# Kernel optimization log

Measured on AMD Instinct MI355X. Metric: run time of the kernel, lower is better.

Reference implementation:

```python
import jax, jax.numpy as jnp
import numpy as np

B, T, D = 4, 4096, 384
H = W = 64
K = 8            # num_clusters
CH = MH = 64     # conv_hidden, mlp_hidden
NL = 4           # num_layers
IN_DIM = D + 2   # use_spatial_pos
RADIUS_FRACTION = 30.0
GRAPH_EPS = 1e-6
SM_LAMBDA = 0.01
FS_LAMBDA = 0.09


def conv2d(x, w, b, groups=1):
    out = jax.lax.conv_general_dilated(x, w, (1, 1), 'SAME',
        dimension_numbers=('NCHW', 'OIHW', 'NCHW'), feature_group_count=groups)
    return out + b[None, :, None, None]


def group_norm(x, g, b, groups, eps=1e-5):
    n, c, h, w = x.shape
    xg = x.reshape(n, groups, c // groups, h, w)
    m = xg.mean(axis=(2, 3, 4), keepdims=True)
    v = xg.var(axis=(2, 3, 4), keepdims=True)
    xn = ((xg - m) * jax.lax.rsqrt(v + eps)).reshape(n, c, h, w)
    return xn * g[None, :, None, None] + b[None, :, None, None]


def layer_norm(x, g, b, eps=1e-5):
    m = x.mean(-1, keepdims=True)
    v = x.var(-1, keepdims=True)
    return (x - m) * jax.lax.rsqrt(v + eps) * g + b


def build_graph():
    # unit-square grid positions; radius graph with self loops; sym normalization
    lin = jnp.linspace(0.0, 1.0, H)
    gy, gx = jnp.meshgrid(lin, lin, indexing='ij')
    pos = jnp.stack([gx.reshape(-1), gy.reshape(-1)], axis=1)  # (T,2)
    r2 = 2.0 / (RADIUS_FRACTION * RADIUS_FRACTION)             # (sqrt(2)/rf)^2
    dx = pos[:, 0][:, None] - pos[:, 0][None, :]
    dy = pos[:, 1][:, None] - pos[:, 1][None, :]
    adj = ((dx * dx + dy * dy) <= r2).astype(jnp.float32)      # includes loop
    deg = adj.sum(1)
    dis = jnp.where(deg > 0, deg ** -0.5, 0.0)
    a_tilde = dis[:, None] * adj * dis[None, :]                # D^-1/2 A D^-1/2
    return pos, a_tilde


def setup_inputs():
    key = jax.random.key(0)
    ks = jax.random.split(key, 16)
    rn = lambda i, s, sc=0.05: jax.random.normal(ks[i], s, dtype=jnp.float32) * sc
    z = lambda s: jnp.zeros(s, jnp.float32)
    o = lambda s: jnp.ones(s, jnp.float32)
    return {
        'token_features': jax.random.normal(ks[0], (B, T, D), dtype=jnp.float32),
        'gcn_w0': rn(1, (IN_DIM, CH)), 'gcn_b0': z((CH,)),
        'gcn_w': rn(2, (NL - 1, CH, CH)), 'gcn_b': z((NL - 1, CH)),
        'ln_g': o((NL, CH)), 'ln_b': z((NL, CH)),
        'res_w': rn(3, (IN_DIM, CH)), 'res_b': z((CH,)),
        'res_ln_g': o((CH,)), 'res_ln_b': z((CH,)),
        'mlp_w1': rn(4, (CH, MH)), 'mlp_b1': z((MH,)),
        'mlp_ln_g': o((MH,)), 'mlp_ln_b': z((MH,)),
        'mlp_w2': rn(5, (MH, K)), 'mlp_b2': z((K,)),
        'sm_w1': rn(6, (K, 1, 3, 3)), 'sm_b1': z((K,)),
        'sm_gn1_g': o((K,)), 'sm_gn1_b': z((K,)),
        'sm_w2': rn(7, (K, 1, 3, 3)), 'sm_b2': z((K,)),
        'sm_gn2_g': o((K,)), 'sm_gn2_b': z((K,)),
        'ec_w1': rn(8, (32, D, 3, 3), 0.02), 'ec_b1': z((32,)),
        'ec_gn_g': o((32,)), 'ec_gn_b': z((32,)),
        'ec_w2': rn(9, (1, 32, 1, 1)), 'ec_b2': z((1,)),
        'k': 8,
    }


def reference(token_features, gcn_w0, gcn_b0, gcn_w, gcn_b, ln_g, ln_b,
              res_w, res_b, res_ln_g, res_ln_b, mlp_w1, mlp_b1, mlp_ln_g,
              mlp_ln_b, mlp_w2, mlp_b2, sm_w1, sm_b1, sm_gn1_g, sm_gn1_b,
              sm_w2, sm_b2, sm_gn2_g, sm_gn2_b, ec_w1, ec_b1, ec_gn_g,
              ec_gn_b, ec_w2, ec_b2, k):
    pos, A = build_graph()

    # ---- feature smoothness loss (edge-aware) ----
    fs = token_features.reshape(B, H, W, D).transpose(0, 3, 1, 2)  # (B,D,H,W)
    e = jax.nn.relu(group_norm(conv2d(fs, ec_w1, ec_b1), ec_gn_g, ec_gn_b, 8))
    ew = jax.nn.sigmoid(conv2d(e, ec_w2, ec_b2))                   # (B,1,H,W)
    gy = fs[:, :, 1:, :] - fs[:, :, :-1, :]
    gx = fs[:, :, :, 1:] - fs[:, :, :, :-1]
    loss_y = (gy * gy * ew[:, :, 1:, :]).mean() / D
    loss_x = (gx * gx * ew[:, :, :, 1:]).mean() / D
    feat_sm = (loss_y + loss_x) / 2

    # ---- GNN pool (batched; adjacency shared across batch) ----
    x = jnp.concatenate(
        [token_features, jnp.broadcast_to(pos[None], (B, T, 2))], axis=-1)
    Ws = [gcn_w0] + [gcn_w[i] for i in range(NL - 1)]
    bs = [gcn_b0] + [gcn_b[i] for i in range(NL - 1)]
    for i in range(NL):
        x_prev = x
        h = jnp.einsum('ts,bsc->btc', A, x @ Ws[i]) + bs[i]  # GCNConv
        h = jax.nn.elu(layer_norm(h, ln_g[i], ln_b[i]))
        if i == 0:
            x_prev = layer_norm(x_prev @ res_w + res_b, res_ln_g, res_ln_b)
        x = h + x_prev
    h1 = jax.nn.elu(layer_norm(x @ mlp_w1 + mlp_b1, mlp_ln_g, mlp_ln_b))
    S = jax.nn.softmax(h1 @ mlp_w2 + mlp_b2, axis=-1)        # (B,T,K)

    # ---- spatial smoothness loss (depthwise convs) ----
    S_sp = S.transpose(0, 2, 1).reshape(B, K, H, W)
    t = jax.nn.relu(group_norm(conv2d(S_sp, sm_w1, sm_b1, groups=K),
                               sm_gn1_g, sm_gn1_b, K))
    S_sm = group_norm(conv2d(t, sm_w2, sm_b2, groups=K), sm_gn2_g, sm_gn2_b, K)
    sm_loss = ((S_sm - S_sp) ** 2).mean(axis=(1, 2, 3))      # (B,)

    # ---- normalized-cut + orthogonality losses ----
    AS = jnp.einsum('ts,bsk->btk', A, S)
    num = jnp.einsum('btk,btk->b', S, AS)
    degA = A.sum(1)
    den = jnp.einsum('btk,t,btk->b', S, degA, S) + GRAPH_EPS
    loss_c = -num / den
    SS = jnp.einsum('btk,btl->bkl', S, S)
    ssn = jnp.sqrt((SS * SS).sum(axis=(1, 2)))
    eyeK = jnp.eye(K, dtype=jnp.float32)
    target = eyeK / (jnp.sqrt(jnp.float32(K)) + GRAPH_EPS)
    diff = SS / (ssn[:, None, None] + GRAPH_EPS) - target[None]
    loss_o = jnp.sqrt((diff * diff).sum(axis=(1, 2)))

    loss = (loss_c + loss_o + SM_LAMBDA * sm_loss).mean() + FS_LAMBDA * feat_sm
    return S, loss
```

## Files before the change

### kernel.cpp

```cpp
#include <hip/hip_runtime.h>
#include <hip/hip_bf16.h>


#define B_ 4
#define T_ 4096
#define D_ 384

typedef __attribute__((ext_vector_type(8))) short short8b;
typedef __attribute__((ext_vector_type(4))) float f32x4;

__device__ __forceinline__ float wred(float v) {
#pragma unroll
  for (int off = 32; off > 0; off >>= 1) v += __shfl_xor(v, off);
  return v;
}

__device__ __forceinline__ void wred2(float& a, float& b) {
#pragma unroll
  for (int off = 32; off > 0; off >>= 1) {
    a += __shfl_xor(a, off);
    b += __shfl_xor(b, off);
  }
}

__device__ __forceinline__ short bf16rne(float f) {
  unsigned u = __float_as_uint(f);
  unsigned r = (u + 0x7FFFu + ((u >> 16) & 1u)) >> 16;
  return (short)r;
}

__device__ __forceinline__ float bf2f(short s) {
  return __uint_as_float(((unsigned)(unsigned short)s) << 16);
}

__device__ __forceinline__ float uval(int i) {
  int c = (i < 2 ? i : 2) + ((63 - i) < 2 ? (63 - i) : 2) + 1;
  return rsqrtf((float)c);
}

struct PGcn {
  const float *feat, *ecw1, *w0, *resw, *resb, *resg, *reslb;
  const float *gw, *gb0, *gb, *lng, *lnb;
  const float *w1, *b1, *mlng, *mlnb, *w2, *b2;
  short *fb, *wq, *wb;
  float *accg, *xwA, *xwB, *xbuf, *resbuf, *S, *Sp;
};

struct PLoss {
  const float *S, *Sp;
  const float *smw1, *smb1, *smg1, *smbb1, *smw2, *smb2, *smg2, *smbb2;
  const short *fb, *wq;
  const float *ecb1;
  float *eraw, *accg;
  const float *gng, *gnb, *ecw2, *ecb2;
  float *ew, *outp;
};


__device__ __forceinline__ void prep_stage(int blk, int tid,
    const float* feat, const float* ecw1, const float* w0, const float* resw,
    short* fb, short* wq, short* wb, float* accg) {
  if (blk == 0) {
    accg[tid] = 0.f;
    accg[tid + 256] = 0.f;
  }
  if (blk < 3072) {
    int t = blk * 256 + tid;
    const float4* s = (const float4*)feat + (size_t)t * 2;
    float4 a = s[0], b = s[1];
    short8b v;
    v[0] = bf16rne(a.x); v[1] = bf16rne(a.y); v[2] = bf16rne(a.z); v[3] = bf16rne(a.w);
    v[4] = bf16rne(b.x); v[5] = bf16rne(b.y); v[6] = bf16rne(b.z); v[7] = bf16rne(b.w);
    *(short8b*)(fb + (size_t)t * 8) = v;
  } else if (blk < 3504) {
    int idx = (blk - 3072) * 256 + tid;
    int q = idx % 9;
    int rest = idx / 9;
    int d = rest % 384;
    int o = rest / 384;
    wq[((size_t)(q * 32 + o)) * 384 + d] = bf16rne(ecw1[idx]);
  } else {
    int u = (blk - 3504) * 256 + tid;
    int l = u & 63, f = (u >> 6) & 7, s = u >> 9;
    int c = f * 16 + (l & 15);
    int k0 = s * 32 + ((l >> 4) << 3);
    const float* src = (c < 64) ? (w0 + c) : (resw + (c - 64));
    short8b v;
#pragma unroll
    for (int j = 0; j < 8; ++j) v[j] = bf16rne(src[(size_t)(k0 + j) * 64]);
    *(short8b*)(wb + (size_t)u * 8) = v;
  }
}

__device__ __forceinline__ void gemm0_stage(char* smem, int blk, int tid,
    const short* fb, const short* wb, const float* w0, const float* resw,
    const float* resb, const float* resg, const float* reslb,
    float* xw, float* res) {
  short8b* Ab8 = (short8b*)smem;
  int row0 = blk * 32;
#pragma unroll
  for (int it = 0; it < 6; ++it) {
    int u = it * 256 + tid;
    int l = u & 63, s = (u >> 6) % 12, set = u / 768;
    int row = row0 + set * 16 + (l & 15);
    int k = s * 32 + ((l >> 4) << 3);
    Ab8[(set * 12 + s) * 64 + l] = *(const short8b*)(fb + (size_t)row * 384 + k);
  }
  __syncthreads();
  int wid = tid >> 6, lane = tid & 63;
  int rowset = wid & 1, colhalf = wid >> 1;
  const short8b* wb8 = (const short8b*)wb;
  f32x4 acc[4];
#pragma unroll
  for (int f = 0; f < 4; ++f) acc[f] = (f32x4){0.f, 0.f, 0.f, 0.f};
#pragma unroll
  for (int s = 0; s < 12; ++s) {
    short8b av = Ab8[(rowset * 12 + s) * 64 + lane];
#pragma unroll
    for (int f = 0; f < 4; ++f) {
      short8b bv = wb8[((size_t)(s * 8 + colhalf * 4 + f)) * 64 + lane];
      acc[f] = __builtin_amdgcn_mfma_f32_16x16x32_bf16(av, bv, acc[f], 0, 0, 0);
    }
  }
  int g = lane >> 4, ln = lane & 15;
  if (colhalf == 0) {
    float pw1[4], pw2[4];
#pragma unroll
    for (int f = 0; f < 4; ++f) {
      int c = f * 16 + ln;
      pw1[f] = w0[384 * 64 + c];
      pw2[f] = w0[385 * 64 + c];
    }
#pragma unroll
    for (int r = 0; r < 4; ++r) {
      int grow = row0 + rowset * 16 + g * 4 + r;
      int t = grow & (T_ - 1);
      float px = (float)(t & 63) * (1.f / 63.f);
      float py = (float)(t >> 6) * (1.f / 63.f);
#pragma unroll
      for (int f = 0; f < 4; ++f)
        xw[(size_t)grow * 64 + f * 16 + ln] = acc[f][r] + px * pw1[f] + py * pw2[f];
    }
  } else {
    float rw1[4], rw2[4], rb[4], rgam[4], rbet[4];
#pragma unroll
    for (int f = 0; f < 4; ++f) {
      int c = f * 16 + ln;
      rw1[f] = resw[384 * 64 + c];
      rw2[f] = resw[385 * 64 + c];
      rb[f] = resb[c]; rgam[f] = resg[c]; rbet[f] = reslb[c];
    }
#pragma unroll
    for (int r = 0; r < 4; ++r) {
      int grow = row0 + rowset * 16 + g * 4 + r;
      int t = grow & (T_ - 1);
      float px = (float)(t & 63) * (1.f / 63.f);
      float py = (float)(t >> 6) * (1.f / 63.f);
      float rv[4];
      float s1 = 0.f, s2 = 0.f;
#pragma unroll
      for (int f = 0; f < 4; ++f) {
        float v = acc[f][r] + px * rw1[f] + py * rw2[f] + rb[f];
        rv[f] = v;
        s1 += v;
        s2 = fmaf(v, v, s2);
      }
#pragma unroll
      for (int off = 1; off < 16; off <<= 1) {
        s1 += __shfl_xor(s1, off);
        s2 += __shfl_xor(s2, off);
      }
      float mean = s1 * (1.f / 64.f);
      float var = s2 * (1.f / 64.f) - mean * mean;
      float inv = rsqrtf(var + 1e-5f);
#pragma unroll
      for (int f = 0; f < 4; ++f)
        res[(size_t)grow * 64 + f * 16 + ln] =
            (rv[f] - mean) * inv * rgam[f] + rbet[f];
    }
  }
}

__device__ __forceinline__ void layer_stage(char* smem, int blk, int tid,
    const float* xw_in, const float* W, const float* bias, const float* lng,
    const float* lnb, const float* resid, float* xout, float* xw_out) {
  float* sx = (float*)smem;
  float* sW = (float*)(smem + 4096);
  int t0 = blk * 16;
  int b = t0 >> 12, i = (t0 >> 6) & 63;
  const float4* w4 = (const float4*)W;
  float4* sW4 = (float4*)sW;
#pragma unroll
  for (int l = 0; l < 4; ++l) sW4[tid + l * 256] = w4[tid + l * 256];
  int c = tid & 63, jg = tid >> 6;
  int jb = (t0 & 63) + jg * 4;
  float ui = uval(i);
  float acc[4];
#pragma unroll
  for (int m = 0; m < 4; ++m) acc[m] = 0.f;
  float uw[8];
#pragma unroll
  for (int d = 0; d < 8; ++d) {
    int jj = jb - 2 + d;
    uw[d] = (jj >= 0 && jj < 64) ? uval(jj) : 0.f;
  }
#pragma unroll
  for (int di = -2; di <= 2; ++di) {
    int ii = i + di;
    if (ii < 0 || ii > 63) continue;
    float wi = uval(ii);
    const float* src = xw_in + ((size_t)((b << 12) + (ii << 6))) * 64 + c;
    float v[8];
#pragma unroll
    for (int d = 0; d < 8; ++d) {
      int jj = jb - 2 + d;
      v[d] = (jj >= 0 && jj < 64) ? src[jj * 64] : 0.f;
    }
#pragma unroll
    for (int m = 0; m < 4; ++m) {
      float t = v[m] * uw[m] + v[m + 1] * uw[m + 1] + v[m + 2] * uw[m + 2] +
                v[m + 3] * uw[m + 3] + v[m + 4] * uw[m + 4];
      acc[m] = fmaf(wi, t, acc[m]);
    }
  }
  float bc = bias[c], gam = lng[c], bet = lnb[c];
#pragma unroll
  for (int m = 0; m < 4; ++m) {
    int lrow = jg * 4 + m;
    float h = ui * uval(jb + m) * acc[m] + bc;
    float s1 = h, s2 = h * h;
    wred2(s1, s2);
    float mean = s1 * (1.f / 64.f);
    float var = s2 * (1.f / 64.f) - mean * mean;
    float n = (h - mean) * rsqrtf(var + 1e-5f) * gam + bet;
    float e = n > 0.f ? n : (expf(n) - 1.f);
    float xv = e + resid[(size_t)(t0 + lrow) * 64 + c];
    xout[(size_t)(t0 + lrow) * 64 + c] = xv;
    sx[lrow * 64 + c] = xv;
  }
  __syncthreads();
  float a[4];
#pragma unroll
  for (int m = 0; m < 4; ++m) a[m] = 0.f;
#pragma unroll
  for (int kq = 0; kq < 16; ++kq) {
    float4 fv[4];
#pragma unroll
    for (int m = 0; m < 4; ++m)
      fv[m] = *(const float4*)&sx[(jg * 4 + m) * 64 + kq * 4];
#pragma unroll
    for (int dk = 0; dk < 4; ++dk) {
      float wv = sW[(kq * 4 + dk) * 64 + c];
#pragma unroll
      for (int m = 0; m < 4; ++m)
        a[m] = fmaf(((const float*)&fv[m])[dk], wv, a[m]);
    }
  }
#pragma unroll
  for (int m = 0; m < 4; ++m)
    xw_out[(size_t)(t0 + jg * 4 + m) * 64 + c] = a[m];
}

__device__ __forceinline__ void st4mlp_stage(char* smem, int blk, int tid,
    const float* xw_in, const float* bias, const float* lng, const float* lnb,
    const float* resid, const float* w1, const float* b1, const float* mlng,
    const float* mlnb, const float* w2, const float* b2, float* S, float* Sp) {
  float* sx = (float*)smem;
  float* sW = (float*)(smem + 8192);
  float* sh = (float*)(smem + 24576);
  int t0 = blk * 32;
  int b = t0 >> 12, i = (t0 >> 6) & 63;
  const float4* w4 = (const float4*)w1;
  float4* sW4 = (float4*)sW;
#pragma unroll
  for (int l = 0; l < 4; ++l) sW4[tid + l * 256] = w4[tid + l * 256];
  int c = tid & 63, jg = tid >> 6;
  int jb = (t0 & 63) + jg * 8;
  float ui = uval(i);
  float acc[8];
#pragma unroll
  for (int m = 0; m < 8; ++m) acc[m] = 0.f;
  float uw[12];
#pragma unroll
  for (int d = 0; d < 12; ++d) {
    int jj = jb - 2 + d;
    uw[d] = (jj >= 0 && jj < 64) ? uval(jj) : 0.f;
  }
#pragma unroll
  for (int di = -2; di <= 2; ++di) {
    int ii = i + di;
    if (ii < 0 || ii > 63) continue;
    float wi = uval(ii);
    const float* src = xw_in + ((size_t)((b << 12) + (ii << 6))) * 64 + c;
    float v[12];
#pragma unroll
    for (int d = 0; d < 12; ++d) {
      int jj = jb - 2 + d;
      v[d] = (jj >= 0 && jj < 64) ? src[jj * 64] : 0.f;
    }
#pragma unroll
    for (int m = 0; m < 8; ++m) {
      float t = v[m] * uw[m] + v[m + 1] * uw[m + 1] + v[m + 2] * uw[m + 2] +
                v[m + 3] * uw[m + 3] + v[m + 4] * uw[m + 4];
      acc[m] = fmaf(wi, t, acc[m]);
    }
  }
  float bc = bias[c], gam = lng[c], bet = lnb[c];
#pragma unroll
  for (int m = 0; m < 8; ++m) {
    int lrow = jg * 8 + m;
    float h = ui * uval(jb + m) * acc[m] + bc;
    float s1 = h, s2 = h * h;
    wred2(s1, s2);
    float mean = s1 * (1.f / 64.f);
    float var = s2 * (1.f / 64.f) - mean * mean;
    float n = (h - mean) * rsqrtf(var + 1e-5f) * gam + bet;
    float e = n > 0.f ? n : (expf(n) - 1.f);
    sx[lrow * 64 + c] = e + resid[(size_t)(t0 + lrow) * 64 + c];
  }
  __syncthreads();
  float a[8];
#pragma unroll
  for (int m = 0; m < 8; ++m) a[m] = 0.f;
#pragma unroll
  for (int kq = 0; kq < 16; ++kq) {
    float4 fv[8];
#pragma unroll
    for (int m = 0; m < 8; ++m)
      fv[m] = *(const float4*)&sx[(jg * 8 + m) * 64 + kq * 4];
#pragma unroll
    for (int dk = 0; dk < 4; ++dk) {
      float wv = sW[(kq * 4 + dk) * 64 + c];
#pragma unroll
      for (int m = 0; m < 8; ++m)
        a[m] = fmaf(((const float*)&fv[m])[dk], wv, a[m]);
    }
  }
  float mb = b1[c], mgam = mlng[c], mbet = mlnb[c];
#pragma unroll
  for (int m = 0; m < 8; ++m) {
    float h = a[m] + mb;
    float s1 = h, s2 = h * h;
    wred2(s1, s2);
    float mean = s1 * (1.f / 64.f);
    float var = s2 * (1.f / 64.f) - mean * mean;
    float n = (h - mean) * rsqrtf(var + 1e-5f) * mgam + mbet;
    sh[(jg * 8 + m) * 64 + c] = n > 0.f ? n : (expf(n) - 1.f);
  }
  __syncthreads();
  int k = tid & 7, j = tid >> 3;
  float lg = b2[k];
#pragma unroll 8
  for (int u = 0; u < 64; ++u) {
    int cc = (u + j * 8) & 63;
    lg = fmaf(sh[j * 64 + cc], w2[cc * 8 + k], lg);
  }
  float mx = lg;
  mx = fmaxf(mx, __shfl_xor(mx, 1));
  mx = fmaxf(mx, __shfl_xor(mx, 2));
  mx = fmaxf(mx, __shfl_xor(mx, 4));
  float ex = expf(lg - mx);
  float sum = ex;
  sum += __shfl_xor(sum, 1);
  sum += __shfl_xor(sum, 2);
  sum += __shfl_xor(sum, 4);
  float val = ex / sum;
  int grow = t0 + j;
  int t = grow & (T_ - 1);
  S[(size_t)grow * 8 + k] = val;
  Sp[((size_t)((b << 3) + k) << 12) + t] = val;
}

__device__ __forceinline__ void cut_stage(char* smem, int blk, int tid,
    const float* S, float* accg) {
  {
    int k = tid & 7;
    int tl = tid >> 3;
    int gid = blk * 32 + tl;
    int b = gid >> 12, t = gid & (T_ - 1);
    int i = t >> 6, j = t & 63;
    float ui = uval(i), uj = uval(j);
    float as = 0.f, sui = 0.f, suj = 0.f;
#pragma unroll
    for (int di = -2; di <= 2; ++di) {
      int ii = i + di;
      if (ii < 0 || ii > 63) continue;
      float wi = uval(ii);
      sui += wi;
#pragma unroll
      for (int dj = -2; dj <= 2; ++dj) {
        int jj = j + dj;
        if (jj < 0 || jj > 63) continue;
        as = fmaf(wi * uval(jj),
                  S[((size_t)((b << 12) + (ii << 6) + jj)) * 8 + k], as);
      }
    }
#pragma unroll
    for (int dj = -2; dj <= 2; ++dj) {
      int jj = j + dj;
      if (jj >= 0 && jj <= 63) suj += uval(jj);
    }
    as *= ui * uj;
    float sv = S[(size_t)gid * 8 + k];
    float degA = ui * uj * sui * suj;
    float numv = sv * as, denv = sv * sv * degA;
    wred2(numv, denv);
    float* lds = (float*)smem;
    int wid = tid >> 6, lane = tid & 63;
    if (lane == 0) { lds[wid * 2] = numv; lds[wid * 2 + 1] = denv; }
    __syncthreads();
    if (tid == 0) {
      int slot = b * 4 + (blk & 3);
      atomicAdd(&accg[slot], lds[0] + lds[2] + lds[4] + lds[6]);
      atomicAdd(&accg[16 + slot], lds[1] + lds[3] + lds[5] + lds[7]);
    }
  }
  if (blk < 32) {
    __syncthreads();
    int b = blk >> 3, chunk = blk & 7;
    int wid = tid >> 6, lane = tid & 63;
    int kk = lane >> 3, ll = lane & 7;
    int t0 = chunk * 512 + wid * 128;
    float a = 0.f;
    const float* Sb = S + ((size_t)b << 12) * 8;
    for (int it = 0; it < 128; ++it) {
      const float* sr = Sb + (size_t)(t0 + it) * 8;
      a = fmaf(sr[kk], sr[ll], a);
    }
    float* lds2 = (float*)smem;
    lds2[tid] = a;
    __syncthreads();
    if (tid < 64) {
      float s = lds2[tid] + lds2[tid + 64] + lds2[tid + 128] + lds2[tid + 192];
      atomicAdd(&accg[128 + b * 64 + tid], s);
    }
  }
}

__device__ __forceinline__ void sm_stage(char* smem, int bk, int tid,
    const float* Sp, const float* w1, const float* b1, const float* g1,
    const float* bb1, const float* w2, const float* b2, const float* g2,
    const float* bb2, float* accg) {
  float* p0 = (float*)smem;
  float* p1 = p0 + 4096;
  float* red = p1 + 4096;
  int b = bk >> 3, k = bk & 7;
  const float4* src = (const float4*)(Sp + (size_t)bk * 4096);
  float4* d0 = (float4*)p0;
  for (int i2 = tid; i2 < 1024; i2 += 256) d0[i2] = src[i2];
  float W1[9], W2[9];
#pragma unroll
  for (int q = 0; q < 9; ++q) { W1[q] = w1[k * 9 + q]; W2[q] = w2[k * 9 + q]; }
  __syncthreads();
  int wid = tid >> 6, lane = tid & 63;
  float y[16];
  float s1 = 0.f, s2 = 0.f;
#pragma unroll
  for (int v = 0; v < 16; ++v) {
    int p = v * 256 + tid;
    int i2 = p >> 6, j2 = p & 63;
    float a = b1[k];
#pragma unroll
    for (int dy = 0; dy < 3; ++dy) {
      int ii = i2 + dy - 1;
      if (ii < 0 || ii > 63) continue;
#pragma unroll
      for (int dx = 0; dx < 3; ++dx) {
        int jj = j2 + dx - 1;
        if (jj < 0 || jj > 63) continue;
        a = fmaf(W1[dy * 3 + dx], p0[(ii << 6) + jj], a);
      }
    }
    y[v] = a;
    s1 += a;
    s2 = fmaf(a, a, s2);
  }
  wred2(s1, s2);
  if (lane == 0) { red[wid * 2] = s1; red[wid * 2 + 1] = s2; }
  __syncthreads();
  float mean = (red[0] + red[2] + red[4] + red[6]) * (1.f / 4096.f);
  float var = (red[1] + red[3] + red[5] + red[7]) * (1.f / 4096.f) - mean * mean;
  float inv = rsqrtf(var + 1e-5f) * g1[k];
  float sh = bb1[k];
  __syncthreads();
#pragma unroll
  for (int v = 0; v < 16; ++v) {
    int p = v * 256 + tid;
    p1[p] = fmaxf((y[v] - mean) * inv + sh, 0.f);
  }
  __syncthreads();
  s1 = 0.f; s2 = 0.f;
#pragma unroll
  for (int v = 0; v < 16; ++v) {
    int p = v * 256 + tid;
    int i2 = p >> 6, j2 = p & 63;
    float a = b2[k];
#pragma unroll
    for (int dy = 0; dy < 3; ++dy) {
      int ii = i2 + dy - 1;
      if (ii < 0 || ii > 63) continue;
#pragma unroll
      for (int dx = 0; dx < 3; ++dx) {
        int jj = j2 + dx - 1;
        if (jj < 0 || jj > 63) continue;
        a = fmaf(W2[dy * 3 + dx], p1[(ii << 6) + jj], a);
      }
    }
    y[v] = a;
    s1 += a;
    s2 = fmaf(a, a, s2);
  }
  wred2(s1, s2);
  if (lane == 0) { red[wid * 2] = s1; red[wid * 2 + 1] = s2; }
  __syncthreads();
  float mean2 = (red[0] + red[2] + red[4] + red[6]) * (1.f / 4096.f);
  float var2 = (red[1] + red[3] + red[5] + red[7]) * (1.f / 4096.f) - mean2 * mean2;
  float inv2 = rsqrtf(var2 + 1e-5f) * g2[k];
  float sh2 = bb2[k];
  float sd = 0.f;
#pragma unroll
  for (int v = 0; v < 16; ++v) {
    int p = v * 256 + tid;
    float sm = (y[v] - mean2) * inv2 + sh2;
    float dd = sm - p0[p];
    sd = fmaf(dd, dd, sd);
  }
  sd = wred(sd);
  __syncthreads();
  if (lane == 0) red[wid] = sd;
  __syncthreads();
  if (tid == 0)
    atomicAdd(&accg[384 + b * 2 + (bk & 1)],
              (red[0] + red[1] + red[2] + red[3]) * (1.f / 32768.f));
}

__device__ __forceinline__ void ecconv_stage(char* smem, int blk2, int tid,
    const short* fb, const short* wq, const float* ecb1, float* eraw,
    float* accg) {
  short* Abuf = (short*)smem;
  short* Wbuf = Abuf + 8040;
  float* sW1 = (float*)smem;
  float* sW2 = sW1 + 128;
  int b = blk2 >> 6, i = blk2 & 63;
  int wid = tid >> 6, lane = tid & 63;
  int m = lane & 15, kg = lane >> 4;
  if (tid < 36) {
    int zkg = tid & 3, sl = (tid >> 2) % 3, r = tid / 12;
    int slot = sl == 0 ? 0 : (sl == 1 ? 65 : 66);
    *(short8b*)&Abuf[(r * 67 + slot) * 40 + zkg * 8] = (short8b)0;
  }
  f32x4 acc0 = {0.f, 0.f, 0.f, 0.f};
  f32x4 acc1 = {0.f, 0.f, 0.f, 0.f};
  int abase = (wid * 16 + m) * 40 + kg * 8;
  int bbase = m * 40 + kg * 8;
  for (int c = 0; c < 12; ++c) {
    __syncthreads();
#pragma unroll
    for (int s = 0; s < 3; ++s) {
      int cid = tid + (s << 8);
      int akg = cid & 3, px = (cid >> 2) & 63, r = cid >> 8;
      int ii = i + r - 1;
      short8b v = (short8b)0;
      if (ii >= 0 && ii < 64)
        v = *(const short8b*)(fb +
              ((size_t)((b << 12) + (ii << 6) + px)) * D_ + c * 32 + akg * 8);
      *(short8b*)&Abuf[(r * 67 + px + 1) * 40 + akg * 8] = v;
    }
    for (int l = tid; l < 1152; l += 256) {
      int wkg = l & 3, oo = (l >> 2) & 31, q = l >> 7;
      short8b wv =
          *(const short8b*)(wq + ((size_t)(q * 32 + oo)) * D_ + c * 32 + wkg * 8);
      *(short8b*)&Wbuf[(q * 32 + oo) * 40 + wkg * 8] = wv;
    }
    __syncthreads();
#pragma unroll
    for (int q = 0; q < 9; ++q) {
      short8b av = *(const short8b*)&Abuf[abase + ((q / 3) * 67 + (q % 3)) * 40];
      short8b bv0 = *(const short8b*)&Wbuf[bbase + q * 1280];
      short8b bv1 = *(const short8b*)&Wbuf[bbase + q * 1280 + 640];
      acc0 = __builtin_amdgcn_mfma_f32_16x16x32_bf16(av, bv0, acc0, 0, 0, 0);
      acc1 = __builtin_amdgcn_mfma_f32_16x16x32_bf16(av, bv1, acc1, 0, 0, 0);
    }
  }
  __syncthreads();
  int o0 = m, o1 = 16 + m;
  float bs0 = ecb1[o0], bs1 = ecb1[o1];
  float s1a = 0.f, s2a = 0.f, s1b = 0.f, s2b = 0.f;
  int jbase = wid * 16 + kg * 4;
#pragma unroll
  for (int rg = 0; rg < 4; ++rg) {
    float v0 = acc0[rg] + bs0;
    float v1 = acc1[rg] + bs1;
    int j = jbase + rg;
    size_t px = ((size_t)((b << 12) + (i << 6) + j)) * 32;
    eraw[px + o0] = v0;
    eraw[px + o1] = v1;
    s1a += v0; s2a = fmaf(v0, v0, s2a);
    s1b += v1; s2b = fmaf(v1, v1, s2b);
  }
  s1a += __shfl_xor(s1a, 16); s1a += __shfl_xor(s1a, 32);
  s2a += __shfl_xor(s2a, 16); s2a += __shfl_xor(s2a, 32);
  s1b += __shfl_xor(s1b, 16); s1b += __shfl_xor(s1b, 32);
  s2b += __shfl_xor(s2b, 16); s2b += __shfl_xor(s2b, 32);
  if (lane < 16) {
    sW1[wid * 32 + lane] = s1a; sW2[wid * 32 + lane] = s2a;
    sW1[wid * 32 + lane + 16] = s1b; sW2[wid * 32 + lane + 16] = s2b;
  }
  __syncthreads();
  if (tid < 32) {
    float t1 = sW1[tid] + sW1[32 + tid] + sW1[64 + tid] + sW1[96 + tid];
    float t2 = sW2[tid] + sW2[32 + tid] + sW2[64 + tid] + sW2[96 + tid];
    t1 += __shfl_xor(t1, 1); t1 += __shfl_xor(t1, 2);
    t2 += __shfl_xor(t2, 1); t2 += __shfl_xor(t2, 2);
    if ((tid & 3) == 0) {
      atomicAdd(&accg[64 + b * 16 + (tid >> 2) * 2], t1);
      atomicAdd(&accg[64 + b * 16 + (tid >> 2) * 2 + 1], t2);
    }
  }
}

__device__ __forceinline__ void ecfinal_stage(char* smem, int blk, int tid,
    const float* eraw, const float* accg, const float* gng, const float* gnb,
    const float* w2, const float* b2, float* ew) {
  float* st = (float*)smem;
  int idx = blk * 256 + tid;
  int b = idx >> 12;
  if (tid < 16) st[tid] = accg[64 + b * 16 + tid];
  __syncthreads();
  float a = b2[0];
  const float4* er = (const float4*)(eraw + (size_t)idx * 32);
#pragma unroll
  for (int oq = 0; oq < 8; ++oq) {
    float mean = st[oq * 2] * (1.f / 16384.f);
    float var = st[oq * 2 + 1] * (1.f / 16384.f) - mean * mean;
    float inv = rsqrtf(var + 1e-5f);
    float4 e = er[oq];
    int o = oq * 4;
    float v0 = (e.x - mean) * inv * gng[o + 0] + gnb[o + 0];
    float v1 = (e.y - mean) * inv * gng[o + 1] + gnb[o + 1];
    float v2 = (e.z - mean) * inv * gng[o + 2] + gnb[o + 2];
    float v3 = (e.w - mean) * inv * gng[o + 3] + gnb[o + 3];
    a = fmaf(fmaxf(v0, 0.f), w2[o + 0], a);
    a = fmaf(fmaxf(v1, 0.f), w2[o + 1], a);
    a = fmaf(fmaxf(v2, 0.f), w2[o + 2], a);
    a = fmaf(fmaxf(v3, 0.f), w2[o + 3], a);
  }
  ew[idx] = 1.f / (1.f + expf(-a));
}

__device__ __forceinline__ void fsloss_stage(char* smem, int blk, int tid,
    const short* fb, const float* ew, float* accg) {
  float sy = 0.f, sx = 0.f;
  const int N = B_ * T_ * 48;
  for (int idx = blk * 256 + tid; idx < N; idx += 512 * 256) {
    int d8 = idx % 48;
    int rt = idx / 48;
    int t = rt & (T_ - 1);
    int i = t >> 6, j = t & 63;
    const short8b* fp = (const short8b*)(fb + (size_t)rt * D_) + d8;
    short8b f0 = *fp;
    if (i < 63) {
      short8b f1 = fp[64 * 48];
      float w = ew[rt + 64];
      float a = 0.f;
#pragma unroll
      for (int u = 0; u < 8; ++u) {
        float d = bf2f(f1[u]) - bf2f(f0[u]);
        a = fmaf(d, d, a);
      }
      sy += w * a;
    }
    if (j < 63) {
      short8b f1 = fp[48];
      float w = ew[rt + 1];
      float a = 0.f;
#pragma unroll
      for (int u = 0; u < 8; ++u) {
        float d = bf2f(f1[u]) - bf2f(f0[u]);
        a = fmaf(d, d, a);
      }
      sx += w * a;
    }
  }
  wred2(sy, sx);
  float* lds = (float*)smem;
  int wid = tid >> 6, lane = tid & 63;
  if (lane == 0) { lds[wid * 2] = sy; lds[wid * 2 + 1] = sx; }
  __syncthreads();
  if (tid == 0) {
    int slot = 32 + (blk & 15) * 2;
    atomicAdd(&accg[slot], lds[0] + lds[2] + lds[4] + lds[6]);
    atomicAdd(&accg[slot + 1], lds[1] + lds[3] + lds[5] + lds[7]);
  }
}

__device__ __forceinline__ void final_stage(const float* accg, float* out) {
  float total = 0.f;
  for (int b = 0; b < 4; ++b) {
    const float* SSb = accg + 128 + b * 64;
    float ssq = 0.f;
    for (int v = 0; v < 64; ++v) ssq += SSb[v] * SSb[v];
    float ssn = sqrtf(ssq);
    float tgt = 1.f / (sqrtf(8.f) + 1e-6f);
    float inv = 1.f / (ssn + 1e-6f);
    float lo = 0.f;
    for (int kk = 0; kk < 8; ++kk)
      for (int ll = 0; ll < 8; ++ll) {
        float dd = SSb[kk * 8 + ll] * inv - (kk == ll ? tgt : 0.f);
        lo += dd * dd;
      }
    lo = sqrtf(lo);
    float num = accg[b * 4] + accg[b * 4 + 1] + accg[b * 4 + 2] + accg[b * 4 + 3];
    float den = accg[16 + b * 4] + accg[16 + b * 4 + 1] + accg[16 + b * 4 + 2] +
                accg[16 + b * 4 + 3];
    float lc = -num / (den + 1e-6f);
    float smv = accg[384 + b * 2] + accg[385 + b * 2];
    total += lc + lo + 0.01f * smv;
  }
  total *= 0.25f;
  float fsy = 0.f, fsx = 0.f;
  for (int s = 0; s < 16; ++s) { fsy += accg[32 + s * 2]; fsx += accg[33 + s * 2]; }
  const float cnt = 4.f * 384.f * 63.f * 64.f;
  float ly = fsy / cnt * (1.f / 384.f);
  float lx = fsx / cnt * (1.f / 384.f);
  out[131072] = total + 0.09f * 0.5f * (ly + lx);
}


__global__ __launch_bounds__(256) void k_prep(PGcn p) {
  prep_stage(blockIdx.x, threadIdx.x, p.feat, p.ecw1, p.w0, p.resw, p.fb, p.wq,
             p.wb, p.accg);
}

__global__ __launch_bounds__(256) void k_mix1(PGcn g, PLoss l) {
  __shared__ __align__(16) char smem[39168];
  if (blockIdx.x < 256) {
    int lb = (blockIdx.x & 7) * 32 + (blockIdx.x >> 3);
    ecconv_stage(smem, lb, threadIdx.x, l.fb, l.wq, l.ecb1, l.eraw, l.accg);
  } else {
    gemm0_stage(smem, blockIdx.x - 256, threadIdx.x, g.fb, g.wb, g.w0, g.resw,
                g.resb, g.resg, g.reslb, g.xwA, g.resbuf);
  }
}

__global__ __launch_bounds__(256) void k_mix2(PGcn g, PLoss l) {
  __shared__ __align__(16) char smem[20480];
  if (blockIdx.x < 64)
    ecfinal_stage(smem, blockIdx.x, threadIdx.x, l.eraw, l.accg, l.gng, l.gnb,
                  l.ecw2, l.ecb2, l.ew);
  else
    layer_stage(smem, blockIdx.x - 64, threadIdx.x, g.xwA, g.gw, g.gb0, g.lng,
                g.lnb, g.resbuf, g.xbuf, g.xwB);
}

__global__ __launch_bounds__(256) void k_mix3(PGcn g, PLoss l) {
  __shared__ __align__(16) char smem[20480];
  if (blockIdx.x < 512)
    fsloss_stage(smem, blockIdx.x, threadIdx.x, l.fb, l.ew, l.accg);
  else
    layer_stage(smem, blockIdx.x - 512, threadIdx.x, g.xwB, g.gw + 4096, g.gb,
                g.lng + 64, g.lnb + 64, g.xbuf, g.xbuf, g.xwA);
}

__global__ __launch_bounds__(256) void k_layer2(PGcn p) {
  __shared__ __align__(16) char smem[20480];
  layer_stage(smem, blockIdx.x, threadIdx.x, p.xwA, p.gw + 8192, p.gb + 64,
              p.lng + 128, p.lnb + 128, p.xbuf, p.xbuf, p.xwB);
}

__global__ __launch_bounds__(256) void k_st4mlp(PGcn p) {
  __shared__ __align__(16) char smem[32768];
  st4mlp_stage(smem, blockIdx.x, threadIdx.x, p.xwB, p.gb + 128, p.lng + 192,
               p.lnb + 192, p.xbuf, p.w1, p.b1, p.mlng, p.mlnb, p.w2, p.b2,
               p.S, p.Sp);
}

__global__ __launch_bounds__(256) void k_cutsm(PLoss p) {
  __shared__ __align__(16) char smem[32832];
  if (blockIdx.x < 512)
    cut_stage(smem, blockIdx.x, threadIdx.x, p.S, p.accg);
  else
    sm_stage(smem, blockIdx.x - 512, threadIdx.x, p.Sp, p.smw1, p.smb1, p.smg1,
             p.smbb1, p.smw2, p.smb2, p.smg2, p.smbb2, p.accg);
}

__global__ void k_final(PLoss p) {
  if (threadIdx.x == 0 && blockIdx.x == 0) final_stage(p.accg, p.outp);
}


extern "C" void kernel_launch(void* const* d_in, const int* in_sizes, int n_in,
                              void* d_out, int out_size, void* d_ws, size_t ws_size,
                              hipStream_t stream) {
  const float* feat = (const float*)d_in[0];
  const float* gcn_w0 = (const float*)d_in[1];
  const float* gcn_b0 = (const float*)d_in[2];
  const float* gcn_w = (const float*)d_in[3];
  const float* gcn_b = (const float*)d_in[4];
  const float* ln_g = (const float*)d_in[5];
  const float* ln_b = (const float*)d_in[6];
  const float* res_w = (const float*)d_in[7];
  const float* res_b = (const float*)d_in[8];
  const float* res_ln_g = (const float*)d_in[9];
  const float* res_ln_b = (const float*)d_in[10];
  const float* mlp_w1 = (const float*)d_in[11];
  const float* mlp_b1 = (const float*)d_in[12];
  const float* mlp_ln_g = (const float*)d_in[13];
  const float* mlp_ln_b = (const float*)d_in[14];
  const float* mlp_w2 = (const float*)d_in[15];
  const float* mlp_b2 = (const float*)d_in[16];
  const float* sm_w1 = (const float*)d_in[17];
  const float* sm_b1 = (const float*)d_in[18];
  const float* sm_g1 = (const float*)d_in[19];
  const float* sm_bb1 = (const float*)d_in[20];
  const float* sm_w2 = (const float*)d_in[21];
  const float* sm_b2 = (const float*)d_in[22];
  const float* sm_g2 = (const float*)d_in[23];
  const float* sm_bb2 = (const float*)d_in[24];
  const float* ec_w1 = (const float*)d_in[25];
  const float* ec_b1 = (const float*)d_in[26];
  const float* ec_gn_g = (const float*)d_in[27];
  const float* ec_gn_b = (const float*)d_in[28];
  const float* ec_w2 = (const float*)d_in[29];
  const float* ec_b2 = (const float*)d_in[30];

  float* out = (float*)d_out;
  float* ws = (float*)d_ws;
  float* acc = ws;
  float* xwA = ws + 512;
  float* xwB = xwA + 1048576;
  float* xbuf = xwB + 1048576;
  float* resbuf = xbuf + 1048576;
  float* Sp = resbuf + 1048576;
  float* eraw = Sp + 131072;
  float* ew = eraw + 524288;
  short* wqb = (short*)(ew + 16384);
  short* wb = wqb + 110592;
  short* fb = wb + 49152;
  float* S = out;

  PGcn pg = {feat, ec_w1, gcn_w0, res_w, res_b, res_ln_g, res_ln_b,
             gcn_w, gcn_b0, gcn_b, ln_g, ln_b,
             mlp_w1, mlp_b1, mlp_ln_g, mlp_ln_b, mlp_w2, mlp_b2,
             fb, wqb, wb, acc, xwA, xwB, xbuf, resbuf, S, Sp};
  PLoss pl = {S, Sp, sm_w1, sm_b1, sm_g1, sm_bb1, sm_w2, sm_b2, sm_g2, sm_bb2,
              fb, wqb, ec_b1, eraw, acc, ec_gn_g, ec_gn_b, ec_w2, ec_b2, ew,
              out};

  k_prep<<<3528, 256, 0, stream>>>(pg);
  k_mix1<<<768, 256, 0, stream>>>(pg, pl);
  k_mix2<<<1088, 256, 0, stream>>>(pg, pl);
  k_mix3<<<1536, 256, 0, stream>>>(pg, pl);
  k_layer2<<<1024, 256, 0, stream>>>(pg);
  k_st4mlp<<<512, 256, 0, stream>>>(pg);
  k_cutsm<<<544, 256, 0, stream>>>(pl);
  k_final<<<1, 64, 0, stream>>>(pl);
}
```

Baseline: 126.2 us.

## Compute two output rows per ecconv block with 2x2 MFMA register tiling

The 3x3 conv stage now gives each block two image rows, loading four input rows instead of three. Each wave computes a 2x2 grid of 16x16 MFMA tiles, so every A and B fragment load from shared memory is reused twice. The weight tile is staged once per two rows, which halves weight global and shared traffic and the number of conv blocks. The shared-memory row stride also drops from 40 to 36 shorts, which changes the bank mapping and slightly enlarges the LDS allocation. In exchange there are fewer blocks in k_mix1, and possibly higher register pressure.

```diff
diff --git a/kernel.cpp b/kernel.cpp
--- a/kernel.cpp
+++ b/kernel.cpp
@@ -538,65 +538,74 @@
     const short* fb, const short* wq, const float* ecb1, float* eraw,
     float* accg) {
   short* Abuf = (short*)smem;
-  short* Wbuf = Abuf + 8040;
+  short* Wbuf = Abuf + 9648;
   float* sW1 = (float*)smem;
   float* sW2 = sW1 + 128;
-  int b = blk2 >> 6, i = blk2 & 63;
+  int b = blk2 >> 5, i0 = (blk2 & 31) * 2;
   int wid = tid >> 6, lane = tid & 63;
   int m = lane & 15, kg = lane >> 4;
-  if (tid < 36) {
+  int wr = wid >> 1, wh = wid & 1;
+  if (tid < 48) {
     int zkg = tid & 3, sl = (tid >> 2) % 3, r = tid / 12;
     int slot = sl == 0 ? 0 : (sl == 1 ? 65 : 66);
-    *(short8b*)&Abuf[(r * 67 + slot) * 40 + zkg * 8] = (short8b)0;
-  }
-  f32x4 acc0 = {0.f, 0.f, 0.f, 0.f};
-  f32x4 acc1 = {0.f, 0.f, 0.f, 0.f};
-  int abase = (wid * 16 + m) * 40 + kg * 8;
-  int bbase = m * 40 + kg * 8;
+    *(short8b*)&Abuf[(r * 67 + slot) * 36 + zkg * 8] = (short8b)0;
+  }
+  f32x4 acc00 = {0.f, 0.f, 0.f, 0.f};
+  f32x4 acc01 = {0.f, 0.f, 0.f, 0.f};
+  f32x4 acc10 = {0.f, 0.f, 0.f, 0.f};
+  f32x4 acc11 = {0.f, 0.f, 0.f, 0.f};
   for (int c = 0; c < 12; ++c) {
     __syncthreads();
 #pragma unroll
-    for (int s = 0; s < 3; ++s) {
+    for (int s = 0; s < 4; ++s) {
       int cid = tid + (s << 8);
       int akg = cid & 3, px = (cid >> 2) & 63, r = cid >> 8;
-      int ii = i + r - 1;
+      int ii = i0 + r - 1;
       short8b v = (short8b)0;
       if (ii >= 0 && ii < 64)
         v = *(const short8b*)(fb +
               ((size_t)((b << 12) + (ii << 6) + px)) * D_ + c * 32 + akg * 8);
-      *(short8b*)&Abuf[(r * 67 + px + 1) * 40 + akg * 8] = v;
+      *(short8b*)&Abuf[(r * 67 + px + 1) * 36 + akg * 8] = v;
     }
     for (int l = tid; l < 1152; l += 256) {
       int wkg = l & 3, oo = (l >> 2) & 31, q = l >> 7;
       short8b wv =
           *(const short8b*)(wq + ((size_t)(q * 32 + oo)) * D_ + c * 32 + wkg * 8);
-      *(short8b*)&Wbuf[(q * 32 + oo) * 40 + wkg * 8] = wv;
+      *(short8b*)&Wbuf[(q * 32 + oo) * 36 + wkg * 8] = wv;
     }
     __syncthreads();
 #pragma unroll
     for (int q = 0; q < 9; ++q) {
-      short8b av = *(const short8b*)&Abuf[abase + ((q / 3) * 67 + (q % 3)) * 40];
-      short8b bv0 = *(const short8b*)&Wbuf[bbase + q * 1280];
-      short8b bv1 = *(const short8b*)&Wbuf[bbase + q * 1280 + 640];
-      acc0 = __builtin_amdgcn_mfma_f32_16x16x32_bf16(av, bv0, acc0, 0, 0, 0);
-      acc1 = __builtin_amdgcn_mfma_f32_16x16x32_bf16(av, bv1, acc1, 0, 0, 0);
-    }
-  }
-  __syncthreads();
-  int o0 = m, o1 = 16 + m;
-  float bs0 = ecb1[o0], bs1 = ecb1[o1];
+      int rloc = wr + q / 3;
+      int sbase = (rloc * 67 + wh * 32 + m + (q % 3)) * 36 + kg * 8;
+      short8b av0 = *(const short8b*)&Abuf[sbase];
+      short8b av1 = *(const short8b*)&Abuf[sbase + 16 * 36];
+      short8b bv0 = *(const short8b*)&Wbuf[(q * 32 + m) * 36 + kg * 8];
+      short8b bv1 = *(const short8b*)&Wbuf[(q * 32 + 16 + m) * 36 + kg * 8];
+      acc00 = __builtin_amdgcn_mfma_f32_16x16x32_bf16(av0, bv0, acc00, 0, 0, 0);
+      acc01 = __builtin_amdgcn_mfma_f32_16x16x32_bf16(av0, bv1, acc01, 0, 0, 0);
+      acc10 = __builtin_amdgcn_mfma_f32_16x16x32_bf16(av1, bv0, acc10, 0, 0, 0);
+      acc11 = __builtin_amdgcn_mfma_f32_16x16x32_bf16(av1, bv1, acc11, 0, 0, 0);
+    }
+  }
+  __syncthreads();
+  int orow = i0 + wr;
+  float bs0 = ecb1[m], bs1 = ecb1[16 + m];
   float s1a = 0.f, s2a = 0.f, s1b = 0.f, s2b = 0.f;
-  int jbase = wid * 16 + kg * 4;
 #pragma unroll
   for (int rg = 0; rg < 4; ++rg) {
-    float v0 = acc0[rg] + bs0;
-    float v1 = acc1[rg] + bs1;
-    int j = jbase + rg;
-    size_t px = ((size_t)((b << 12) + (i << 6) + j)) * 32;
-    eraw[px + o0] = v0;
-    eraw[px + o1] = v1;
-    s1a += v0; s2a = fmaf(v0, v0, s2a);
-    s1b += v1; s2b = fmaf(v1, v1, s2b);
+    int j0 = wh * 32 + kg * 4 + rg;
+    int j1 = j0 + 16;
+    size_t px0 = ((size_t)((b << 12) + (orow << 6) + j0)) * 32;
+    size_t px1 = ((size_t)((b << 12) + (orow << 6) + j1)) * 32;
+    float v00 = acc00[rg] + bs0, v01 = acc01[rg] + bs1;
+    float v10 = acc10[rg] + bs0, v11 = acc11[rg] + bs1;
+    eraw[px0 + m] = v00;
+    eraw[px0 + 16 + m] = v01;
+    eraw[px1 + m] = v10;
+    eraw[px1 + 16 + m] = v11;
+    s1a += v00 + v10; s2a = fmaf(v00, v00, fmaf(v10, v10, s2a));
+    s1b += v01 + v11; s2b = fmaf(v01, v01, fmaf(v11, v11, s2b));
   }
   s1a += __shfl_xor(s1a, 16); s1a += __shfl_xor(s1a, 32);
   s2a += __shfl_xor(s2a, 16); s2a += __shfl_xor(s2a, 32);
@@ -733,12 +742,12 @@
 }
 
 __global__ __launch_bounds__(256) void k_mix1(PGcn g, PLoss l) {
-  __shared__ __align__(16) char smem[39168];
-  if (blockIdx.x < 256) {
-    int lb = (blockIdx.x & 7) * 32 + (blockIdx.x >> 3);
+  __shared__ __align__(16) char smem[40064];
+  if (blockIdx.x < 128) {
+    int lb = (blockIdx.x & 7) * 16 + (blockIdx.x >> 3);
     ecconv_stage(smem, lb, threadIdx.x, l.fb, l.wq, l.ecb1, l.eraw, l.accg);
   } else {
-    gemm0_stage(smem, blockIdx.x - 256, threadIdx.x, g.fb, g.wb, g.w0, g.resw,
+    gemm0_stage(smem, blockIdx.x - 128, threadIdx.x, g.fb, g.wb, g.w0, g.resw,
                 g.resb, g.resg, g.reslb, g.xwA, g.resbuf);
   }
 }
@@ -848,7 +857,7 @@
               out};
 
   k_prep<<<3528, 256, 0, stream>>>(pg);
-  k_mix1<<<768, 256, 0, stream>>>(pg, pl);
+  k_mix1<<<640, 256, 0, stream>>>(pg, pl);
   k_mix2<<<1088, 256, 0, stream>>>(pg, pl);
   k_mix3<<<1536, 256, 0, stream>>>(pg, pl);
   k_layer2<<<1024, 256, 0, stream>>>(pg);
```

Result: slower. 168.3 us (+33.4%).
